# Kernel tuning notes

Measured on AMD Instinct MI355X. Metric: run time of the kernel, lower is better.

The kernel has to match this reference:

```python
import jax, jax.numpy as jnp
import numpy as np


def _gcn_conv(x, edge_index, W, b):
    """PyG-style GCNConv: h = x @ W; out = D^-1/2 (A+I) D^-1/2 h + b."""
    N = x.shape[0]
    h = x @ W  # [N, F_out]
    # add self loops
    loops = jnp.arange(N, dtype=edge_index.dtype)
    src = jnp.concatenate([edge_index[0], loops])  # [E+N]
    dst = jnp.concatenate([edge_index[1], loops])  # [E+N]
    # symmetric normalization based on in-degree (incl. self loops)
    deg = jnp.zeros((N,), dtype=h.dtype).at[dst].add(1.0)
    dinv = jnp.where(deg > 0, jax.lax.rsqrt(deg), 0.0)
    norm = dinv[src] * dinv[dst]  # [E+N]
    # gather -> scale -> scatter-add
    msgs = h[src] * norm[:, None]  # [E+N, F_out]
    out = jax.ops.segment_sum(msgs, dst, num_segments=N)
    return out + b


def setup_inputs() -> dict:
    key = jax.random.key(0)
    k1, k2, k3, k4 = jax.random.split(key, 4)
    N, E, Cin, Ch, Cout = 50000, 800000, 128, 128, 64
    x = jax.random.normal(k1, (N, Cin), dtype=jnp.float32)
    edge_index = jax.random.randint(k2, (2, E), 0, N, dtype=jnp.int64)
    W1 = jax.random.normal(k3, (Cin, Ch), dtype=jnp.float32) / np.sqrt(Cin)
    b1 = jnp.zeros((Ch,), dtype=jnp.float32)
    W2 = jax.random.normal(k4, (Ch, Cout), dtype=jnp.float32) / np.sqrt(Ch)
    b2 = jnp.zeros((Cout,), dtype=jnp.float32)
    return {"x": x, "edge_index": edge_index, "W1": W1, "b1": b1, "W2": W2, "b2": b2}


def reference(x, edge_index, W1, b1, W2, b2):
    h = jax.nn.relu(_gcn_conv(x, edge_index, W1, b1))
    # F.dropout(training=self.training): eval mode -> identity
    return _gcn_conv(h, edge_index, W2, b2)
```

## Files before the change

kernel.cpp:

```cpp
#include <hip/hip_runtime.h>

typedef _Float16 f16;
typedef f16 f16x2 __attribute__((ext_vector_type(2)));
typedef f16 f16x4 __attribute__((ext_vector_type(4)));
typedef f16 f16x8 __attribute__((ext_vector_type(8)));
typedef float f32x4 __attribute__((ext_vector_type(4)));
typedef int int4a __attribute__((ext_vector_type(4), aligned(4)));

#define BSH 7
#define BN 128
#define CHUNK 4096
#define LCAP 4096
#define NBMAX 512
#define PMAX 512

__global__ __launch_bounds__(256) void degh(const int* __restrict__ dst, int* __restrict__ histG,
                                            const float* __restrict__ W1,
                                            const float* __restrict__ W2, f16* __restrict__ w1t,
                                            f16* __restrict__ w2t, int E, int NB, int nblk) {
    const int t = threadIdx.x, blk = blockIdx.x;
    if (blk < nblk) {
        __shared__ int hist[NBMAX];
        for (int i = t; i < NB; i += 256) hist[i] = 0;
        __syncthreads();
        int lo = blk * CHUNK, hi = min(lo + CHUNK, E);
        for (int i = lo + t; i < hi; i += 256) atomicAdd(&hist[dst[i] >> BSH], 1);
        __syncthreads();
        for (int i = t; i < NB; i += 256) histG[(size_t)i * nblk + blk] = hist[i];
        return;
    }
    if (blk == nblk) {
        for (int idx = t; idx < 128 * 128; idx += 256) {
            int n = idx >> 7, k = idx & 127;
            w1t[idx] = (f16)W1[k * 128 + n];
        }
        return;
    }
    for (int idx = t; idx < 64 * 128; idx += 256) {
        int n = idx >> 7, k = idx & 127;
        w2t[idx] = (f16)W2[k * 64 + n];
    }
}

__global__ __launch_bounds__(256) void scanA(int* __restrict__ a, int* __restrict__ bsum, int L) {
    __shared__ int tmp[256];
    int tid = threadIdx.x;
    int i = blockIdx.x * 256 + tid;
    int v = (i < L) ? a[i] : 0;
    tmp[tid] = v;
    __syncthreads();
    for (int o = 1; o < 256; o <<= 1) {
        int t2 = (tid >= o) ? tmp[tid - o] : 0;
        __syncthreads();
        tmp[tid] += t2;
        __syncthreads();
    }
    if (i < L) a[i] = tmp[tid] - v;
    if (tid == 255) bsum[blockIdx.x] = tmp[255];
}

__global__ __launch_bounds__(256) void scanB(int* __restrict__ bsum, int nb2) {
    __shared__ int excl[PMAX];
    __shared__ int work[PMAX];
    const int t = threadIdx.x;
    for (int i = t; i < PMAX; i += 256) work[i] = (i < nb2) ? bsum[i] : 0;
    __syncthreads();
    for (int o = 1; o < PMAX; o <<= 1) {
        for (int i = t; i < PMAX; i += 256) excl[i] = work[i] + ((i >= o) ? work[i - o] : 0);
        __syncthreads();
        for (int i = t; i < PMAX; i += 256) work[i] = excl[i];
        __syncthreads();
    }
    for (int i = t; i < nb2; i += 256) bsum[i] = (i == 0) ? 0 : work[i - 1];
}

__global__ __launch_bounds__(256) void k1(const float* __restrict__ x,
                                          const f16* __restrict__ w1t,
                                          const int* __restrict__ src, const int* __restrict__ dst,
                                          const int* __restrict__ histG,
                                          const int* __restrict__ bsumx,
                                          int* __restrict__ sorted, f16* __restrict__ h, int N,
                                          int E, int NB, int nblk) {
    __shared__ union SM {
        struct {
            f16 aT[64 * 136];
            f16 bT[128 * 136];
        } g;
        struct {
            int ofs[NBMAX];
        } p;
    } sm;
    const int t = threadIdx.x;

    if ((int)blockIdx.x < nblk) {
        const int blk = blockIdx.x;
        for (int i = t; i < NB; i += 256) {
            int idx = i * nblk + blk;
            sm.p.ofs[i] = histG[idx] + bsumx[idx >> 8];
        }
        __syncthreads();
        int lo = blk * CHUNK, hi = min(lo + CHUNK, E);
        for (int i = lo + t; i < hi; i += 256) {
            int d = dst[i];
            int pos = atomicAdd(&sm.p.ofs[d >> BSH], 1);
            sorted[pos] = (src[i] << BSH) | (d & (BN - 1));
        }
        return;
    }

    const int gb = blockIdx.x - nblk;
    const int row0 = gb * 64;
    {
        int r = t >> 2, s = (t & 3) * 32;
        bool ok = (row0 + r) < N;
        const float* xp = x + (size_t)(row0 + r) * 128 + s;
        f16* dp = &sm.g.aT[r * 136 + s];
#pragma unroll
        for (int c = 0; c < 4; ++c) {
            f16x8 hv;
            if (ok) {
                float4 f0 = *(const float4*)(xp + c * 8);
                float4 f1 = *(const float4*)(xp + c * 8 + 4);
                hv[0] = (f16)f0.x; hv[1] = (f16)f0.y; hv[2] = (f16)f0.z; hv[3] = (f16)f0.w;
                hv[4] = (f16)f1.x; hv[5] = (f16)f1.y; hv[6] = (f16)f1.z; hv[7] = (f16)f1.w;
            } else {
#pragma unroll
                for (int j = 0; j < 8; ++j) hv[j] = (f16)0.f;
            }
            *(f16x8*)(dp + c * 8) = hv;
        }
    }
    for (int idx = t; idx < 128 * 16; idx += 256) {
        int n = idx >> 4, c = idx & 15;
        *(f16x8*)&sm.g.bT[n * 136 + c * 8] = *(const f16x8*)&w1t[n * 128 + c * 8];
    }
    __syncthreads();

    const int w = t >> 6, lane = t & 63, m15 = lane & 15, quad = lane >> 4;
    f32x4 acc[8];
#pragma unroll
    for (int c = 0; c < 8; ++c) acc[c] = (f32x4){0.f, 0.f, 0.f, 0.f};
    const f16* ar = &sm.g.aT[(w * 16 + m15) * 136 + quad * 8];
#pragma unroll
    for (int k0 = 0; k0 < 128; k0 += 32) {
        f16x8 a = *(const f16x8*)(ar + k0);
#pragma unroll
        for (int c = 0; c < 8; ++c) {
            f16x8 b = *(const f16x8*)(&sm.g.bT[(c * 16 + m15) * 136 + k0 + quad * 8]);
            acc[c] = __builtin_amdgcn_mfma_f32_16x16x32_f16(a, b, acc[c], 0, 0, 0);
        }
    }
#pragma unroll
    for (int c = 0; c < 8; ++c)
#pragma unroll
        for (int r = 0; r < 4; ++r) {
            int row = row0 + w * 16 + quad * 4 + r;
            if (row < N) h[(size_t)row * 128 + c * 16 + m15] = (f16)acc[c][r];
        }
}

__global__ __launch_bounds__(256) void bucket_build(const int* __restrict__ histG,
                                                    const int* __restrict__ bsumx,
                                                    const int* __restrict__ sorted,
                                                    int* __restrict__ rowstart,
                                                    float* __restrict__ dinv,
                                                    int* __restrict__ csr_src, int N, int E,
                                                    int NB, int nblk) {
    __shared__ int ent[LCAP];
    __shared__ int hist[BN];
    __shared__ int lofs[BN];
    const int b = blockIdx.x, t = threadIdx.x;

    const int i0 = b * nblk;
    const int base = histG[i0] + bsumx[i0 >> 8];
    const int endb = (b == NB - 1) ? E : (histG[i0 + nblk] + bsumx[(i0 + nblk) >> 8]);
    int total = min(endb - base, LCAP);
    if (b == 0 && t == 0) rowstart[N] = E;

    for (int i = t; i < total; i += 256) ent[i] = sorted[base + i];
    if (t < BN) hist[t] = 0;
    __syncthreads();
    for (int i = t; i < total; i += 256) atomicAdd(&hist[ent[i] & (BN - 1)], 1);
    __syncthreads();
    if (t < BN) lofs[t] = hist[t];
    __syncthreads();
    for (int o = 1; o < BN; o <<= 1) {
        int v = (t < BN && t >= o) ? lofs[t - o] : 0;
        __syncthreads();
        if (t < BN) lofs[t] += v;
        __syncthreads();
    }
    if (t < BN) {
        int ex = lofs[t] - hist[t];
        int node = (b << BSH) + t;
        if (node < N) {
            rowstart[node] = base + ex;
            dinv[node] = rsqrtf((float)hist[t] + 1.0f);
        }
        lofs[t] = ex;
    }
    __syncthreads();
    for (int i = t; i < total; i += 256) {
        int e = ent[i];
        int pos = atomicAdd(&lofs[e & (BN - 1)], 1);
        csr_src[base + pos] = e >> BSH;
    }
}

__global__ __launch_bounds__(256) void gather1(const int* __restrict__ rowstart,
                                               const int* __restrict__ csr_src,
                                               const float* __restrict__ dinv,
                                               const f16* __restrict__ h,
                                               const float* __restrict__ b1,
                                               f16* __restrict__ r1, int N) {
    int wid = (blockIdx.x * 256 + threadIdx.x) >> 6;
    int lane = threadIdx.x & 63;
    int sub = lane >> 5, l32 = lane & 31;
    int node = wid * 2 + sub;
    if (node >= N) return;
    int beg = rowstart[node], end = rowstart[node + 1];
    float dn = dinv[node];
    const f16x4* hv = (const f16x4*)h;

    f16x4 sv = hv[(size_t)node * 32 + l32];
    float a0 = dn * (float)sv[0], a1 = dn * (float)sv[1];
    float a2 = dn * (float)sv[2], a3 = dn * (float)sv[3];
    int i = beg;
    for (; i + 8 <= end; i += 8) {
        int4a sA = *(const int4a*)(csr_src + i);
        int4a sB = *(const int4a*)(csr_src + i + 4);
        float w0 = dinv[sA.x], w1 = dinv[sA.y], w2 = dinv[sA.z], w3 = dinv[sA.w];
        float w4 = dinv[sB.x], w5 = dinv[sB.y], w6 = dinv[sB.z], w7 = dinv[sB.w];
        f16x4 v0 = hv[(size_t)sA.x * 32 + l32];
        f16x4 v1 = hv[(size_t)sA.y * 32 + l32];
        f16x4 v2 = hv[(size_t)sA.z * 32 + l32];
        f16x4 v3 = hv[(size_t)sA.w * 32 + l32];
        f16x4 v4 = hv[(size_t)sB.x * 32 + l32];
        f16x4 v5 = hv[(size_t)sB.y * 32 + l32];
        f16x4 v6 = hv[(size_t)sB.z * 32 + l32];
        f16x4 v7 = hv[(size_t)sB.w * 32 + l32];
        a0 = fmaf(w0, (float)v0[0], a0); a1 = fmaf(w0, (float)v0[1], a1);
        a2 = fmaf(w0, (float)v0[2], a2); a3 = fmaf(w0, (float)v0[3], a3);
        a0 = fmaf(w1, (float)v1[0], a0); a1 = fmaf(w1, (float)v1[1], a1);
        a2 = fmaf(w1, (float)v1[2], a2); a3 = fmaf(w1, (float)v1[3], a3);
        a0 = fmaf(w2, (float)v2[0], a0); a1 = fmaf(w2, (float)v2[1], a1);
        a2 = fmaf(w2, (float)v2[2], a2); a3 = fmaf(w2, (float)v2[3], a3);
        a0 = fmaf(w3, (float)v3[0], a0); a1 = fmaf(w3, (float)v3[1], a1);
        a2 = fmaf(w3, (float)v3[2], a2); a3 = fmaf(w3, (float)v3[3], a3);
        a0 = fmaf(w4, (float)v4[0], a0); a1 = fmaf(w4, (float)v4[1], a1);
        a2 = fmaf(w4, (float)v4[2], a2); a3 = fmaf(w4, (float)v4[3], a3);
        a0 = fmaf(w5, (float)v5[0], a0); a1 = fmaf(w5, (float)v5[1], a1);
        a2 = fmaf(w5, (float)v5[2], a2); a3 = fmaf(w5, (float)v5[3], a3);
        a0 = fmaf(w6, (float)v6[0], a0); a1 = fmaf(w6, (float)v6[1], a1);
        a2 = fmaf(w6, (float)v6[2], a2); a3 = fmaf(w6, (float)v6[3], a3);
        a0 = fmaf(w7, (float)v7[0], a0); a1 = fmaf(w7, (float)v7[1], a1);
        a2 = fmaf(w7, (float)v7[2], a2); a3 = fmaf(w7, (float)v7[3], a3);
    }
    if (i + 4 <= end) {
        int4a s4 = *(const int4a*)(csr_src + i);
        float w0 = dinv[s4.x], w1 = dinv[s4.y], w2 = dinv[s4.z], w3 = dinv[s4.w];
        f16x4 v0 = hv[(size_t)s4.x * 32 + l32];
        f16x4 v1 = hv[(size_t)s4.y * 32 + l32];
        f16x4 v2 = hv[(size_t)s4.z * 32 + l32];
        f16x4 v3 = hv[(size_t)s4.w * 32 + l32];
        a0 = fmaf(w0, (float)v0[0], a0); a1 = fmaf(w0, (float)v0[1], a1);
        a2 = fmaf(w0, (float)v0[2], a2); a3 = fmaf(w0, (float)v0[3], a3);
        a0 = fmaf(w1, (float)v1[0], a0); a1 = fmaf(w1, (float)v1[1], a1);
        a2 = fmaf(w1, (float)v1[2], a2); a3 = fmaf(w1, (float)v1[3], a3);
        a0 = fmaf(w2, (float)v2[0], a0); a1 = fmaf(w2, (float)v2[1], a1);
        a2 = fmaf(w2, (float)v2[2], a2); a3 = fmaf(w2, (float)v2[3], a3);
        a0 = fmaf(w3, (float)v3[0], a0); a1 = fmaf(w3, (float)v3[1], a1);
        a2 = fmaf(w3, (float)v3[2], a2); a3 = fmaf(w3, (float)v3[3], a3);
        i += 4;
    }
    for (; i < end; ++i) {
        int s = csr_src[i];
        float w = dinv[s];
        f16x4 v = hv[(size_t)s * 32 + l32];
        a0 = fmaf(w, (float)v[0], a0); a1 = fmaf(w, (float)v[1], a1);
        a2 = fmaf(w, (float)v[2], a2); a3 = fmaf(w, (float)v[3], a3);
    }
    float4 bb = ((const float4*)b1)[l32];
    float o0 = dn * fmaxf(fmaf(dn, a0, bb.x), 0.f);
    float o1 = dn * fmaxf(fmaf(dn, a1, bb.y), 0.f);
    float o2 = dn * fmaxf(fmaf(dn, a2, bb.z), 0.f);
    float o3 = dn * fmaxf(fmaf(dn, a3, bb.w), 0.f);
    ((f16x4*)r1)[(size_t)node * 32 + l32] = (f16x4){(f16)o0, (f16)o1, (f16)o2, (f16)o3};
}

__global__ __launch_bounds__(256) void gemm2(const f16* __restrict__ r1,
                                             const f16* __restrict__ w2t, f16* __restrict__ h2,
                                             int N) {
    __shared__ f16 aT[64 * 136];
    __shared__ f16 bT[64 * 136];
    const int t = threadIdx.x;
    const int row0 = blockIdx.x * 64;
    {
        int r = t >> 2, s = (t & 3) * 32;
        bool ok = (row0 + r) < N;
        const f16* rp = r1 + (size_t)(row0 + r) * 128 + s;
        f16* dp = &aT[r * 136 + s];
#pragma unroll
        for (int c = 0; c < 4; ++c) {
            f16x8 hv;
            if (ok) hv = *(const f16x8*)(rp + c * 8);
            else {
#pragma unroll
                for (int j = 0; j < 8; ++j) hv[j] = (f16)0.f;
            }
            *(f16x8*)(dp + c * 8) = hv;
        }
    }
    for (int idx = t; idx < 64 * 16; idx += 256) {
        int n = idx >> 4, c = idx & 15;
        *(f16x8*)&bT[n * 136 + c * 8] = *(const f16x8*)&w2t[n * 128 + c * 8];
    }
    __syncthreads();

    const int w = t >> 6, lane = t & 63, m15 = lane & 15, quad = lane >> 4;
    f32x4 acc[4];
#pragma unroll
    for (int c = 0; c < 4; ++c) acc[c] = (f32x4){0.f, 0.f, 0.f, 0.f};
    const f16* ar = &aT[(w * 16 + m15) * 136 + quad * 8];
#pragma unroll
    for (int k0 = 0; k0 < 128; k0 += 32) {
        f16x8 a = *(const f16x8*)(ar + k0);
#pragma unroll
        for (int c = 0; c < 4; ++c) {
            f16x8 b = *(const f16x8*)(&bT[(c * 16 + m15) * 136 + k0 + quad * 8]);
            acc[c] = __builtin_amdgcn_mfma_f32_16x16x32_f16(a, b, acc[c], 0, 0, 0);
        }
    }
#pragma unroll
    for (int c = 0; c < 4; ++c)
#pragma unroll
        for (int r = 0; r < 4; ++r) {
            int row = row0 + w * 16 + quad * 4 + r;
            if (row < N) h2[(size_t)row * 64 + c * 16 + m15] = (f16)acc[c][r];
        }
}

__global__ __launch_bounds__(256) void gather2(const int* __restrict__ rowstart,
                                               const int* __restrict__ csr_src,
                                               const float* __restrict__ dinv,
                                               const f16* __restrict__ h2,
                                               const float* __restrict__ b2,
                                               float* __restrict__ out, int N) {
    int wid = (blockIdx.x * 256 + threadIdx.x) >> 6;
    int lane = threadIdx.x & 63;
    int q = lane >> 4, l16 = lane & 15;
    int node = wid * 4 + q;
    if (node >= N) return;
    int beg = rowstart[node], end = rowstart[node + 1];
    float dn = dinv[node];
    const f16x4* h2v = (const f16x4*)h2;

    f16x4 sv = h2v[(size_t)node * 16 + l16];
    float a0 = (float)sv[0], a1 = (float)sv[1], a2 = (float)sv[2], a3 = (float)sv[3];
    int i = beg;
    for (; i + 8 <= end; i += 8) {
        int4a sA = *(const int4a*)(csr_src + i);
        int4a sB = *(const int4a*)(csr_src + i + 4);
        f16x4 v0 = h2v[(size_t)sA.x * 16 + l16];
        f16x4 v1 = h2v[(size_t)sA.y * 16 + l16];
        f16x4 v2 = h2v[(size_t)sA.z * 16 + l16];
        f16x4 v3 = h2v[(size_t)sA.w * 16 + l16];
        f16x4 v4 = h2v[(size_t)sB.x * 16 + l16];
        f16x4 v5 = h2v[(size_t)sB.y * 16 + l16];
        f16x4 v6 = h2v[(size_t)sB.z * 16 + l16];
        f16x4 v7 = h2v[(size_t)sB.w * 16 + l16];
        a0 += (float)v0[0]; a1 += (float)v0[1]; a2 += (float)v0[2]; a3 += (float)v0[3];
        a0 += (float)v1[0]; a1 += (float)v1[1]; a2 += (float)v1[2]; a3 += (float)v1[3];
        a0 += (float)v2[0]; a1 += (float)v2[1]; a2 += (float)v2[2]; a3 += (float)v2[3];
        a0 += (float)v3[0]; a1 += (float)v3[1]; a2 += (float)v3[2]; a3 += (float)v3[3];
        a0 += (float)v4[0]; a1 += (float)v4[1]; a2 += (float)v4[2]; a3 += (float)v4[3];
        a0 += (float)v5[0]; a1 += (float)v5[1]; a2 += (float)v5[2]; a3 += (float)v5[3];
        a0 += (float)v6[0]; a1 += (float)v6[1]; a2 += (float)v6[2]; a3 += (float)v6[3];
        a0 += (float)v7[0]; a1 += (float)v7[1]; a2 += (float)v7[2]; a3 += (float)v7[3];
    }
    if (i + 4 <= end) {
        int4a s4 = *(const int4a*)(csr_src + i);
        f16x4 v0 = h2v[(size_t)s4.x * 16 + l16];
        f16x4 v1 = h2v[(size_t)s4.y * 16 + l16];
        f16x4 v2 = h2v[(size_t)s4.z * 16 + l16];
        f16x4 v3 = h2v[(size_t)s4.w * 16 + l16];
        a0 += (float)v0[0]; a1 += (float)v0[1]; a2 += (float)v0[2]; a3 += (float)v0[3];
        a0 += (float)v1[0]; a1 += (float)v1[1]; a2 += (float)v1[2]; a3 += (float)v1[3];
        a0 += (float)v2[0]; a1 += (float)v2[1]; a2 += (float)v2[2]; a3 += (float)v2[3];
        a0 += (float)v3[0]; a1 += (float)v3[1]; a2 += (float)v3[2]; a3 += (float)v3[3];
        i += 4;
    }
    for (; i < end; ++i) {
        int s = csr_src[i];
        f16x4 v = h2v[(size_t)s * 16 + l16];
        a0 += (float)v[0]; a1 += (float)v[1]; a2 += (float)v[2]; a3 += (float)v[3];
    }
    float4 bb = ((const float4*)b2)[l16];
    float4 o;
    o.x = fmaf(dn, a0, bb.x);
    o.y = fmaf(dn, a1, bb.y);
    o.z = fmaf(dn, a2, bb.z);
    o.w = fmaf(dn, a3, bb.w);
    ((float4*)out)[(size_t)node * 16 + l16] = o;
}

extern "C" void kernel_launch(void* const* d_in, const int* in_sizes, int n_in,
                              void* d_out, int out_size, void* d_ws, size_t ws_size,
                              hipStream_t stream) {
    const float* x  = (const float*)d_in[0];
    const int*   ei = (const int*)d_in[1];
    const float* W1 = (const float*)d_in[2];
    const float* b1 = (const float*)d_in[3];
    const float* W2 = (const float*)d_in[4];
    const float* b2 = (const float*)d_in[5];

    const int N = in_sizes[0] / 128;
    const int E = in_sizes[1] / 2;
    const int* src = ei;
    const int* dst = ei + E;
    const int NB   = (N + BN - 1) >> BSH;
    const int nblk = (E + CHUNK - 1) / CHUNK;
    const int L    = NB * nblk;
    const int nb2  = (L + 255) / 256;

    char* p = (char*)d_ws;
    auto bump = [&](size_t bytes) {
        char* r = p;
        p += (bytes + 255) & ~(size_t)255;
        return r;
    };
    int*   histG    = (int*)bump((size_t)L * 4);
    int*   bsum     = (int*)bump((size_t)nb2 * 4);
    int*   sorted   = (int*)bump((size_t)E * 4);
    int*   rowstart = (int*)bump((size_t)(N + 1) * 4);
    float* dinv     = (float*)bump((size_t)N * 4);
    int*   csr_src  = (int*)bump((size_t)E * 4);
    f16*   h        = (f16*)bump((size_t)N * 128 * 2);
    f16*   r1       = (f16*)bump((size_t)N * 128 * 2);
    f16*   h2       = (f16*)bump((size_t)N * 64 * 2);
    f16*   w1t      = (f16*)bump((size_t)128 * 128 * 2);
    f16*   w2t      = (f16*)bump((size_t)64 * 128 * 2);
    float* out      = (float*)d_out;

    degh<<<nblk + 2, 256, 0, stream>>>(dst, histG, W1, W2, w1t, w2t, E, NB, nblk);
    scanA<<<nb2, 256, 0, stream>>>(histG, bsum, L);
    scanB<<<1, 256, 0, stream>>>(bsum, nb2);
    k1<<<nblk + (N + 63) / 64, 256, 0, stream>>>(x, w1t, src, dst, histG, bsum, sorted, h, N, E,
                                                 NB, nblk);
    bucket_build<<<NB, 256, 0, stream>>>(histG, bsum, sorted, rowstart, dinv, csr_src, N, E, NB,
                                         nblk);
    gather1<<<((N + 1) / 2 + 3) / 4, 256, 0, stream>>>(rowstart, csr_src, dinv, h, b1, r1, N);
    gemm2<<<(N + 63) / 64, 256, 0, stream>>>(r1, w2t, h2, N);
    gather2<<<((N + 3) / 4 + 3) / 4, 256, 0, stream>>>(rowstart, csr_src, dinv, h2, b2, out, N);
}
```

Measured before the change: 183.6 us.

## Fold partial scan into consumers and move GEMM1 beside bucket build

Removes the separate scanB launch: each placement block and each bucket-build block redundantly rescans the block partial sums in shared memory. The GEMM1 work moves out of the placement kernel and into the bucket-build kernel, so the x@W1 blocks run alongside CSR construction. CHUNK is doubled, which halves the number of placement and histogram blocks. The aim is fewer launches and a better overlap of the dense GEMM with the sort work. The cost is redundant scan work and syncs in every block, plus a larger shared-memory union in k4.

```diff
diff --git a/kernel.cpp b/kernel.cpp
--- a/kernel.cpp
+++ b/kernel.cpp
@@ -9,7 +9,7 @@
 
 #define BSH 7
 #define BN 128
-#define CHUNK 4096
+#define CHUNK 8192
 #define LCAP 4096
 #define NBMAX 512
 #define PMAX 512
@@ -59,56 +59,107 @@
     if (tid == 255) bsum[blockIdx.x] = tmp[255];
 }
 
-__global__ __launch_bounds__(256) void scanB(int* __restrict__ bsum, int nb2) {
+__device__ __forceinline__ void scan_partials(const int* __restrict__ bsum, int nb2,
+                                              int* excl , int* work ) {
+    const int t = threadIdx.x & 255;
+    for (int i = t; i < PMAX; i += 256) work[i] = (i < nb2) ? bsum[i] : 0;
+    __syncthreads();
+    for (int o = 1; o < PMAX; o <<= 1) {
+        for (int i = t; i < PMAX; i += 256) excl[i] = work[i] + ((i >= o) ? work[i - o] : 0);
+        __syncthreads();
+        for (int i = t; i < PMAX; i += 256) work[i] = excl[i];
+        __syncthreads();
+    }
+    for (int i = t; i < PMAX; i += 256) excl[i] = (i == 0) ? 0 : work[i - 1];
+    __syncthreads();
+}
+
+__global__ __launch_bounds__(256) void placeK(const int* __restrict__ src,
+                                              const int* __restrict__ dst,
+                                              const int* __restrict__ histG,
+                                              const int* __restrict__ bsum, int nb2,
+                                              int* __restrict__ sorted, int E, int NB, int nblk) {
     __shared__ int excl[PMAX];
     __shared__ int work[PMAX];
-    const int t = threadIdx.x;
-    for (int i = t; i < PMAX; i += 256) work[i] = (i < nb2) ? bsum[i] : 0;
-    __syncthreads();
-    for (int o = 1; o < PMAX; o <<= 1) {
-        for (int i = t; i < PMAX; i += 256) excl[i] = work[i] + ((i >= o) ? work[i - o] : 0);
-        __syncthreads();
-        for (int i = t; i < PMAX; i += 256) work[i] = excl[i];
-        __syncthreads();
-    }
-    for (int i = t; i < nb2; i += 256) bsum[i] = (i == 0) ? 0 : work[i - 1];
-}
-
-__global__ __launch_bounds__(256) void k1(const float* __restrict__ x,
-                                          const f16* __restrict__ w1t,
-                                          const int* __restrict__ src, const int* __restrict__ dst,
-                                          const int* __restrict__ histG,
-                                          const int* __restrict__ bsumx,
-                                          int* __restrict__ sorted, f16* __restrict__ h, int N,
-                                          int E, int NB, int nblk) {
+    __shared__ int ofs[NBMAX];
+    const int t = threadIdx.x, blk = blockIdx.x;
+    scan_partials(bsum, nb2, excl, work);
+    for (int i = t; i < NB; i += 256) {
+        int idx = i * nblk + blk;
+        ofs[i] = histG[idx] + excl[idx >> 8];
+    }
+    __syncthreads();
+    int lo = blk * CHUNK, hi = min(lo + CHUNK, E);
+    for (int i = lo + t; i < hi; i += 256) {
+        int d = dst[i];
+        int pos = atomicAdd(&ofs[d >> BSH], 1);
+        sorted[pos] = (src[i] << BSH) | (d & (BN - 1));
+    }
+}
+
+__global__ __launch_bounds__(256) void k4(const int* __restrict__ histG,
+                                          const int* __restrict__ bsum, int nb2,
+                                          const int* __restrict__ sorted,
+                                          int* __restrict__ rowstart, float* __restrict__ dinv,
+                                          int* __restrict__ csr_src, const float* __restrict__ x,
+                                          const f16* __restrict__ w1t, f16* __restrict__ h,
+                                          int N, int E, int NB, int nblk) {
     __shared__ union SM {
         struct {
             f16 aT[64 * 136];
             f16 bT[128 * 136];
         } g;
         struct {
-            int ofs[NBMAX];
-        } p;
+            int ent[LCAP];
+            int hist[BN];
+            int lofs[BN];
+            int excl[PMAX];
+            int work[PMAX];
+        } b;
     } sm;
     const int t = threadIdx.x;
 
-    if ((int)blockIdx.x < nblk) {
-        const int blk = blockIdx.x;
-        for (int i = t; i < NB; i += 256) {
-            int idx = i * nblk + blk;
-            sm.p.ofs[i] = histG[idx] + bsumx[idx >> 8];
-        }
-        __syncthreads();
-        int lo = blk * CHUNK, hi = min(lo + CHUNK, E);
-        for (int i = lo + t; i < hi; i += 256) {
-            int d = dst[i];
-            int pos = atomicAdd(&sm.p.ofs[d >> BSH], 1);
-            sorted[pos] = (src[i] << BSH) | (d & (BN - 1));
+    if ((int)blockIdx.x < NB) {
+        const int b = blockIdx.x;
+        scan_partials(bsum, nb2, sm.b.excl, sm.b.work);
+        const int i0 = b * nblk;
+        const int base = histG[i0] + sm.b.excl[i0 >> 8];
+        const int endb = (b == NB - 1) ? E : (histG[i0 + nblk] + sm.b.excl[(i0 + nblk) >> 8]);
+        int total = min(endb - base, LCAP);
+        if (b == 0 && t == 0) rowstart[N] = E;
+
+        for (int i = t; i < total; i += 256) sm.b.ent[i] = sorted[base + i];
+        if (t < BN) sm.b.hist[t] = 0;
+        __syncthreads();
+        for (int i = t; i < total; i += 256) atomicAdd(&sm.b.hist[sm.b.ent[i] & (BN - 1)], 1);
+        __syncthreads();
+        if (t < BN) sm.b.lofs[t] = sm.b.hist[t];
+        __syncthreads();
+        for (int o = 1; o < BN; o <<= 1) {
+            int v = (t < BN && t >= o) ? sm.b.lofs[t - o] : 0;
+            __syncthreads();
+            if (t < BN) sm.b.lofs[t] += v;
+            __syncthreads();
+        }
+        if (t < BN) {
+            int ex = sm.b.lofs[t] - sm.b.hist[t];
+            int node = (b << BSH) + t;
+            if (node < N) {
+                rowstart[node] = base + ex;
+                dinv[node] = rsqrtf((float)sm.b.hist[t] + 1.0f);
+            }
+            sm.b.lofs[t] = ex;
+        }
+        __syncthreads();
+        for (int i = t; i < total; i += 256) {
+            int e = sm.b.ent[i];
+            int pos = atomicAdd(&sm.b.lofs[e & (BN - 1)], 1);
+            csr_src[base + pos] = e >> BSH;
         }
         return;
     }
 
-    const int gb = blockIdx.x - nblk;
+    const int gb = blockIdx.x - NB;
     const int row0 = gb * 64;
     {
         int r = t >> 2, s = (t & 3) * 32;
@@ -157,54 +208,6 @@
             int row = row0 + w * 16 + quad * 4 + r;
             if (row < N) h[(size_t)row * 128 + c * 16 + m15] = (f16)acc[c][r];
         }
-}
-
-__global__ __launch_bounds__(256) void bucket_build(const int* __restrict__ histG,
-                                                    const int* __restrict__ bsumx,
-                                                    const int* __restrict__ sorted,
-                                                    int* __restrict__ rowstart,
-                                                    float* __restrict__ dinv,
-                                                    int* __restrict__ csr_src, int N, int E,
-                                                    int NB, int nblk) {
-    __shared__ int ent[LCAP];
-    __shared__ int hist[BN];
-    __shared__ int lofs[BN];
-    const int b = blockIdx.x, t = threadIdx.x;
-
-    const int i0 = b * nblk;
-    const int base = histG[i0] + bsumx[i0 >> 8];
-    const int endb = (b == NB - 1) ? E : (histG[i0 + nblk] + bsumx[(i0 + nblk) >> 8]);
-    int total = min(endb - base, LCAP);
-    if (b == 0 && t == 0) rowstart[N] = E;
-
-    for (int i = t; i < total; i += 256) ent[i] = sorted[base + i];
-    if (t < BN) hist[t] = 0;
-    __syncthreads();
-    for (int i = t; i < total; i += 256) atomicAdd(&hist[ent[i] & (BN - 1)], 1);
-    __syncthreads();
-    if (t < BN) lofs[t] = hist[t];
-    __syncthreads();
-    for (int o = 1; o < BN; o <<= 1) {
-        int v = (t < BN && t >= o) ? lofs[t - o] : 0;
-        __syncthreads();
-        if (t < BN) lofs[t] += v;
-        __syncthreads();
-    }
-    if (t < BN) {
-        int ex = lofs[t] - hist[t];
-        int node = (b << BSH) + t;
-        if (node < N) {
-            rowstart[node] = base + ex;
-            dinv[node] = rsqrtf((float)hist[t] + 1.0f);
-        }
-        lofs[t] = ex;
-    }
-    __syncthreads();
-    for (int i = t; i < total; i += 256) {
-        int e = ent[i];
-        int pos = atomicAdd(&lofs[e & (BN - 1)], 1);
-        csr_src[base + pos] = e >> BSH;
-    }
 }
 
 __global__ __launch_bounds__(256) void gather1(const int* __restrict__ rowstart,
@@ -444,11 +447,9 @@
 
     degh<<<nblk + 2, 256, 0, stream>>>(dst, histG, W1, W2, w1t, w2t, E, NB, nblk);
     scanA<<<nb2, 256, 0, stream>>>(histG, bsum, L);
-    scanB<<<1, 256, 0, stream>>>(bsum, nb2);
-    k1<<<nblk + (N + 63) / 64, 256, 0, stream>>>(x, w1t, src, dst, histG, bsum, sorted, h, N, E,
-                                                 NB, nblk);
-    bucket_build<<<NB, 256, 0, stream>>>(histG, bsum, sorted, rowstart, dinv, csr_src, N, E, NB,
-                                         nblk);
+    placeK<<<nblk, 256, 0, stream>>>(src, dst, histG, bsum, nb2, sorted, E, NB, nblk);
+    k4<<<NB + (N + 63) / 64, 256, 0, stream>>>(histG, bsum, nb2, sorted, rowstart, dinv, csr_src,
+                                               x, w1t, h, N, E, NB, nblk);
     gather1<<<((N + 1) / 2 + 3) / 4, 256, 0, stream>>>(rowstart, csr_src, dinv, h, b1, r1, N);
     gemm2<<<(N + 63) / 64, 256, 0, stream>>>(r1, w2t, h2, N);
     gather2<<<((N + 3) / 4 + 3) / 4, 256, 0, stream>>>(rowstart, csr_src, dinv, h2, b2, out, N);
```

After: 191.1 us. +4.1%, slower.
